# Kernel optimization log

Measured on AMD Instinct MI355X. Metric: run time of the kernel, lower is better.

Reference implementation:

```python
import jax, jax.numpy as jnp
import numpy as np

WINDOW = 16  # window_size from init_kwargs


def sigmoid_cutoff(x):
    # max(min(1.2*sigmoid(x) - 0.1, 1), 0)
    return jnp.clip(1.2 * jax.nn.sigmoid(x) - 0.1, 0.0, 1.0)


def setup_inputs() -> dict:
    key = jax.random.key(0)
    k1, k2, k3 = jax.random.split(key, 3)
    B, S, H = 8, 2048, 1024
    x = jax.random.normal(k1, (B, S, H), dtype=jnp.float32)
    # Dense kernels (glorot-ish scale), x_layer has no bias, y_layer has bias
    Wx = jax.random.normal(k2, (H, H), dtype=jnp.float32) * (1.0 / np.sqrt(H))
    Wy = jax.random.normal(k3, (H, 2 * H), dtype=jnp.float32) * (1.0 / np.sqrt(H))
    by = jnp.zeros((2 * H,), dtype=jnp.float32)
    return {"x": x, "Wx": Wx, "Wy": Wy, "by": by}


def reference(x, Wx, Wy, by):
    B, S, H = x.shape
    # left-pad sequence with window_size-1 zeros, then project once (x_layer)
    xp = jnp.pad(x, ((0, 0), (WINDOW - 1, 0), (0, 0)))
    proj = jnp.einsum('bsh,hd->bsd', xp, Wx)  # [B, S+W-1, H]

    def step(state, i):
        # inputs[:, i:S+i] in the original loop
        inp = jax.lax.dynamic_slice_in_dim(proj, i, S, axis=1)  # [B,S,H]
        ns = jnp.einsum('bsh,hd->bsd', state, Wy) + by          # [B,S,2H]
        # reshape [B,S,2,H]: channel 0 = candidate, channel 1 = gate
        cand, gate_logits = jnp.split(ns, 2, axis=-1)
        gate = sigmoid_cutoff(gate_logits)
        new_state = jax.nn.relu(gate * (inp + cand) + (1.0 - gate) * state)
        return new_state, None

    state0 = jnp.zeros_like(x)
    state, _ = jax.lax.scan(step, state0, jnp.arange(WINDOW))
    return state
```

## Files before the change

kernel.cpp:

```cpp
#include <hip/hip_runtime.h>

#define H 1024
#define SEQ 2048
#define MROWS 16384
#define KD 1024
#define NT32 32
#define EPW 72

typedef _Float16 f16;
typedef _Float16 f16x8 __attribute__((ext_vector_type(8)));
typedef float f32x4 __attribute__((ext_vector_type(4)));

__device__ __forceinline__ float gate_fn(float x) {
    float s = 1.0f / (1.0f + __expf(-x));
    return fminf(fmaxf(1.2f * s - 0.1f, 0.0f), 1.0f);
}

__device__ __forceinline__ void gload_lds16(const void* g, void* lds) {
    __builtin_amdgcn_global_load_lds(
        (const __attribute__((address_space(1))) unsigned int*)g,
        (__attribute__((address_space(3))) unsigned int*)lds, 16, 0, 0);
}

__global__ void k_f32_to_f16(const float* __restrict__ in, f16* __restrict__ out) {
    size_t i = ((size_t)blockIdx.x * blockDim.x + threadIdx.x) * 8;
    float4 v0 = *(const float4*)(in + i);
    float4 v1 = *(const float4*)(in + i + 4);
    f16x8 o;
    o[0] = (f16)v0.x; o[1] = (f16)v0.y; o[2] = (f16)v0.z; o[3] = (f16)v0.w;
    o[4] = (f16)v1.x; o[5] = (f16)v1.y; o[6] = (f16)v1.z; o[7] = (f16)v1.w;
    *(f16x8*)(out + i) = o;
}

__global__ void k_transpose_f16(const float* __restrict__ Wsrc, f16* __restrict__ WT,
                                int K, int N) {
    __shared__ float tile[32][33];
    int n0 = blockIdx.x * 32, k0 = blockIdx.y * 32;
    for (int i = threadIdx.y; i < 32; i += 8)
        tile[i][threadIdx.x] = Wsrc[(size_t)(k0 + i) * N + n0 + threadIdx.x];
    __syncthreads();
    for (int i = threadIdx.y; i < 32; i += 8)
        WT[(size_t)(n0 + i) * K + k0 + threadIdx.x] = (f16)tile[threadIdx.x][i];
}

__global__ __launch_bounds__(256) void k_proj_gemm(const f16* __restrict__ A,
                                                   const f16* __restrict__ BT,
                                                   f16* __restrict__ P16) {
    __shared__ alignas(16) f16 Alds[128 * 32];
    __shared__ alignas(16) f16 Blds[128 * 32];
    const int tid = threadIdx.x;
    const int lane = tid & 63, wid = tid >> 6;
    const int l15 = lane & 15, l4 = lane >> 4;
    const int bm = blockIdx.x, bn = blockIdx.y;

    const f16* gA[2]; const f16* gB[2];
    char* ldsA[2]; char* ldsB[2];
#pragma unroll
    for (int it = 0; it < 2; ++it) {
        int c = it * 4 + wid;
        int row = c * 16 + (lane >> 2);
        int kch = (lane & 3) ^ ((row >> 1) & 3);
        gA[it] = A + (size_t)(bm * 128 + row) * KD + kch * 8;
        gB[it] = BT + (size_t)(bn * 128 + row) * KD + kch * 8;
        ldsA[it] = (char*)Alds + c * 1024;
        ldsB[it] = (char*)Blds + c * 1024;
    }

    int offA[2], offB[8];
#pragma unroll
    for (int m = 0; m < 2; ++m) {
        int row = wid * 32 + m * 16 + l15;
        offA[m] = row * 64 + ((l4 ^ ((row >> 1) & 3)) << 4);
    }
#pragma unroll
    for (int n = 0; n < 8; ++n) {
        int row = n * 16 + l15;
        offB[n] = row * 64 + ((l4 ^ ((row >> 1) & 3)) << 4);
    }

    f32x4 acc[2][8] = {};

    for (int kt = 0; kt < KD / 32; ++kt) {
        __syncthreads();
#pragma unroll
        for (int it = 0; it < 2; ++it) {
            gload_lds16(gA[it], ldsA[it]);
            gload_lds16(gB[it], ldsB[it]);
            gA[it] += 32; gB[it] += 32;
        }
        __syncthreads();
        f16x8 a[2], b[8];
#pragma unroll
        for (int m = 0; m < 2; ++m) a[m] = *(const f16x8*)((const char*)Alds + offA[m]);
#pragma unroll
        for (int n = 0; n < 8; ++n) b[n] = *(const f16x8*)((const char*)Blds + offB[n]);
#pragma unroll
        for (int n = 0; n < 8; ++n)
#pragma unroll
            for (int m = 0; m < 2; ++m)
                acc[m][n] = __builtin_amdgcn_mfma_f32_16x16x32_f16(a[m], b[n], acc[m][n], 0, 0, 0);
    }

#pragma unroll
    for (int m = 0; m < 2; ++m)
#pragma unroll
        for (int n = 0; n < 8; ++n) {
            int col = bn * 128 + n * 16 + l15;
#pragma unroll
            for (int r = 0; r < 4; ++r) {
                int row = bm * 128 + wid * 32 + m * 16 + l4 * 4 + r;
                P16[(size_t)row * H + col] = (f16)acc[m][n][r];
            }
        }
}

__global__ void k_step0(const f16* __restrict__ P16, const float* __restrict__ by,
                        f16* __restrict__ S16) {
    size_t idx = ((size_t)blockIdx.x * blockDim.x + threadIdx.x) * 8;
    int row = (int)(idx >> 10);
    int d = (int)(idx & 1023);
    int s = row & (SEQ - 1);
    f16x8 p = {};
    if (s >= 15) p = *(const f16x8*)(P16 + (size_t)(row - 15) * H + d);
    float4 byc0 = *(const float4*)(by + d);
    float4 byc1 = *(const float4*)(by + d + 4);
    float4 byg0 = *(const float4*)(by + H + d);
    float4 byg1 = *(const float4*)(by + H + d + 4);
    f16x8 sv;
#pragma unroll
    for (int j = 0; j < 8; ++j) {
        float byc = (j < 4) ? ((const float*)&byc0)[j] : ((const float*)&byc1)[j - 4];
        float byg = (j < 4) ? ((const float*)&byg0)[j] : ((const float*)&byg1)[j - 4];
        float g = gate_fn(byg);
        float v = fmaxf(g * ((float)p[j] + byc), 0.f);
        sv[j] = (f16)v;
    }
    *(f16x8*)(S16 + idx) = sv;
}

__global__ __launch_bounds__(512, 4) void k_step_gemm(const f16* __restrict__ A,
                                                      const f16* __restrict__ BT,
                                                      const f16* __restrict__ P16,
                                                      const float* __restrict__ by,
                                                      float* __restrict__ Out,
                                                      f16* __restrict__ Snext,
                                                      int stepi) {
    __shared__ alignas(16) char lds[73728];
    const int tid = threadIdx.x;
    const int lane = tid & 63, w = tid >> 6;
    const int l15 = lane & 15, l4 = lane >> 4;
    const int wr = w >> 1, wc = w & 1;

    const int orig = blockIdx.x;
    const int wg = (orig & 7) * 128 + (orig >> 3);
    const int bm = wg >> 4, tb = wg & 15;

    const int rA0 = w * 16 + (lane >> 2), rA1 = rA0 + 128;
    const int slotA = (lane & 3) ^ ((rA0 >> 1) & 3);
    const char* pA0 = (const char*)A + ((size_t)(bm * 256 + rA0) * KD + slotA * 8) * 2;
    const char* pA1 = (const char*)A + ((size_t)(bm * 256 + rA1) * KD + slotA * 8) * 2;
    const int rB = rA0;
    const int rowB = ((rB & 32) ? H : 0) + tb * 64 + ((rB >> 6) << 5) + (rB & 31);
    const int slotB = (lane & 3) ^ ((rB >> 1) & 3);
    const char* pB = (const char*)BT + ((size_t)rowB * KD + slotB * 8) * 2;
    const int dst = w * 1024 + lane * 16;

#define STAGE(bp) do { \
        gload_lds16(pA0, (bp) + dst); \
        gload_lds16(pA1, (bp) + 8192 + dst); \
        gload_lds16(pB,  (bp) + 16384 + dst); \
        pA0 += 64; pA1 += 64; pB += 64; } while (0)

    const int sx = (l4 ^ ((l15 >> 1) & 3)) << 4;
    int offA[4], offB[4];
#pragma unroll
    for (int m = 0; m < 4; ++m) offA[m] = (wr * 64 + m * 16 + l15) * 64 + sx;
#pragma unroll
    for (int n = 0; n < 4; ++n) offB[n] = 16384 + (wc * 64 + n * 16 + l15) * 64 + sx;

    f32x4 acc[4][4] = {};

    char* cb = lds;
    char* nx = lds + 24576;

    STAGE(cb);
    __syncthreads();

    for (int t = 0; t < NT32; ++t) {
        if (t + 1 < NT32) STAGE(nx);
        f16x8 a[4], b[4];
#pragma unroll
        for (int m = 0; m < 4; ++m) a[m] = *(const f16x8*)(cb + offA[m]);
#pragma unroll
        for (int n = 0; n < 4; ++n) b[n] = *(const f16x8*)(cb + offB[n]);
        __builtin_amdgcn_s_setprio(1);
#pragma unroll
        for (int m = 0; m < 4; ++m)
#pragma unroll
            for (int n = 0; n < 4; ++n)
                acc[m][n] = __builtin_amdgcn_mfma_f32_16x16x32_f16(a[m], b[n], acc[m][n], 0, 0, 0);
        __builtin_amdgcn_s_setprio(0);
        __syncthreads();
        char* tmp = cb; cb = nx; nx = tmp;
    }
#undef STAGE

    const bool last = (stepi == 15);
    f16* Cand = (f16*)lds;
    f16* Gate = (f16*)(lds + 36864);
#pragma unroll
    for (int m = 0; m < 4; ++m)
#pragma unroll
        for (int n = 0; n < 2; ++n)
#pragma unroll
            for (int r4 = 0; r4 < 4; ++r4) {
                int row = wr * 64 + m * 16 + l4 * 4 + r4;
                int cc = wc * 32 + n * 16 + l15;
                Cand[row * EPW + cc] = (f16)acc[m][n][r4];
                Gate[row * EPW + cc] = (f16)acc[m][n + 2][r4];
            }
    __syncthreads();
    {
        const int g = tid & 7;
        const int rb = tid >> 3;
        const int dl = g * 8;
        const int d = tb * 64 + dl;
        float4 byc0 = *(const float4*)(by + d);
        float4 byc1 = *(const float4*)(by + d + 4);
        float4 byg0 = *(const float4*)(by + H + d);
        float4 byg1 = *(const float4*)(by + H + d + 4);
#pragma unroll
        for (int p = 0; p < 4; ++p) {
            int row = p * 64 + rb;
            int grow = bm * 256 + row;
            int s = grow & (SEQ - 1);
            f16x8 c8 = *(const f16x8*)(Cand + row * EPW + dl);
            f16x8 g8 = *(const f16x8*)(Gate + row * EPW + dl);
            f16x8 p8 = {};
            if (s >= 15 - stepi)
                p8 = *(const f16x8*)(P16 + (size_t)(grow + stepi - 15) * H + d);
            f16x8 s8 = *(const f16x8*)(A + (size_t)grow * H + d);
            f16x8 o8; float ov[8];
#pragma unroll
            for (int j = 0; j < 8; ++j) {
                float byc = (j < 4) ? ((const float*)&byc0)[j] : ((const float*)&byc1)[j - 4];
                float byg = (j < 4) ? ((const float*)&byg0)[j] : ((const float*)&byg1)[j - 4];
                float cand = (float)c8[j] + byc;
                float gg = gate_fn((float)g8[j] + byg);
                float v = fmaxf(gg * ((float)p8[j] + cand) + (1.f - gg) * (float)s8[j], 0.f);
                o8[j] = (f16)v; ov[j] = v;
            }
            if (!last) {
                *(f16x8*)(Snext + (size_t)grow * H + d) = o8;
            } else {
                *(float4*)(Out + (size_t)grow * H + d) = make_float4(ov[0], ov[1], ov[2], ov[3]);
                *(float4*)(Out + (size_t)grow * H + d + 4) = make_float4(ov[4], ov[5], ov[6], ov[7]);
            }
        }
    }
}

extern "C" void kernel_launch(void* const* d_in, const int* in_sizes, int n_in,
                              void* d_out, int out_size, void* d_ws, size_t ws_size,
                              hipStream_t stream) {
    (void)in_sizes; (void)n_in; (void)out_size; (void)ws_size;
    const float* x  = (const float*)d_in[0];
    const float* Wx = (const float*)d_in[1];
    const float* Wy = (const float*)d_in[2];
    const float* by = (const float*)d_in[3];
    float* out = (float*)d_out;

    char* ws = (char*)d_ws;
    const size_t MB = 1024ull * 1024ull;
    f16* st16a = (f16*)(ws);
    f16* st16b = (f16*)(ws + 32 * MB);
    f16* P16   = (f16*)(ws + 64 * MB);
    f16* WxT   = (f16*)(ws + 96 * MB);
    f16* WyT   = (f16*)(ws + 98 * MB);

    hipLaunchKernelGGL(k_f32_to_f16, dim3(MROWS * H / 8 / 256), dim3(256), 0, stream, x, st16a);
    hipLaunchKernelGGL(k_transpose_f16, dim3(H / 32, H / 32), dim3(32, 8), 0, stream, Wx, WxT, H, H);
    hipLaunchKernelGGL(k_transpose_f16, dim3(2 * H / 32, H / 32), dim3(32, 8), 0, stream, Wy, WyT, H, 2 * H);
    hipLaunchKernelGGL(k_proj_gemm, dim3(MROWS / 128, H / 128), dim3(256), 0, stream, st16a, WxT, P16);
    hipLaunchKernelGGL(k_step0, dim3(MROWS * H / 8 / 256), dim3(256), 0, stream, P16, by, st16b);

    f16* bufs[2] = {st16a, st16b};
    for (int i = 1; i <= 15; ++i) {
        const f16* cur = bufs[i & 1];
        f16* nxt = bufs[(i + 1) & 1];
        hipLaunchKernelGGL(k_step_gemm, dim3(MROWS / 256 * 16), dim3(512), 0, stream,
                           cur, WyT, P16, by, out, nxt, i);
    }
}
```

Baseline: 1.286 ms.

## Load A fragments directly from global into registers, stage only B through LDS

The step GEMM no longer stages the A tile through LDS. Each wave loads its own A fragments straight from global memory into registers, double-buffered as even/odd register sets, and only the B tile goes through LDS via global_load_lds. This cuts LDS traffic and LDS footprint per stage. The cost is that A rows are read redundantly across the two column waves (wc), with less coalesced global access and more VGPR pressure.

```diff
diff --git a/kernel.cpp b/kernel.cpp
--- a/kernel.cpp
+++ b/kernel.cpp
@@ -155,55 +155,72 @@
     const int wg = (orig & 7) * 128 + (orig >> 3);
     const int bm = wg >> 4, tb = wg & 15;
 
-    const int rA0 = w * 16 + (lane >> 2), rA1 = rA0 + 128;
-    const int slotA = (lane & 3) ^ ((rA0 >> 1) & 3);
-    const char* pA0 = (const char*)A + ((size_t)(bm * 256 + rA0) * KD + slotA * 8) * 2;
-    const char* pA1 = (const char*)A + ((size_t)(bm * 256 + rA1) * KD + slotA * 8) * 2;
-    const int rB = rA0;
+    const int rB = tid >> 2;
     const int rowB = ((rB & 32) ? H : 0) + tb * 64 + ((rB >> 6) << 5) + (rB & 31);
-    const int slotB = (lane & 3) ^ ((rB >> 1) & 3);
+    const int slotB = (tid & 3) ^ ((rB >> 1) & 3);
     const char* pB = (const char*)BT + ((size_t)rowB * KD + slotB * 8) * 2;
-    const int dst = w * 1024 + lane * 16;
-
-#define STAGE(bp) do { \
-        gload_lds16(pA0, (bp) + dst); \
-        gload_lds16(pA1, (bp) + 8192 + dst); \
-        gload_lds16(pB,  (bp) + 16384 + dst); \
-        pA0 += 64; pA1 += 64; pB += 64; } while (0)
+
+    const char* ap[4];
+#pragma unroll
+    for (int m = 0; m < 4; ++m)
+        ap[m] = (const char*)A + ((size_t)(bm * 256 + wr * 64 + m * 16 + l15) * KD + l4 * 8) * 2;
+
+#define STAGEB(bp) do { gload_lds16(pB, (bp) + tid * 16); pB += 64; } while (0)
 
     const int sx = (l4 ^ ((l15 >> 1) & 3)) << 4;
-    int offA[4], offB[4];
-#pragma unroll
-    for (int m = 0; m < 4; ++m) offA[m] = (wr * 64 + m * 16 + l15) * 64 + sx;
-#pragma unroll
-    for (int n = 0; n < 4; ++n) offB[n] = 16384 + (wc * 64 + n * 16 + l15) * 64 + sx;
+    int offB[4];
+#pragma unroll
+    for (int n = 0; n < 4; ++n) offB[n] = (wc * 64 + n * 16 + l15) * 64 + sx;
 
     f32x4 acc[4][4] = {};
-
-    char* cb = lds;
-    char* nx = lds + 24576;
-
-    STAGE(cb);
+    f16x8 aE[4], aO[4];
+
+    char* const buf0 = lds;
+    char* const buf1 = lds + 8192;
+
+    STAGEB(buf0);
+#pragma unroll
+    for (int m = 0; m < 4; ++m) { aE[m] = *(const f16x8*)ap[m]; ap[m] += 64; }
     __syncthreads();
 
-    for (int t = 0; t < NT32; ++t) {
-        if (t + 1 < NT32) STAGE(nx);
-        f16x8 a[4], b[4];
-#pragma unroll
-        for (int m = 0; m < 4; ++m) a[m] = *(const f16x8*)(cb + offA[m]);
-#pragma unroll
-        for (int n = 0; n < 4; ++n) b[n] = *(const f16x8*)(cb + offB[n]);
-        __builtin_amdgcn_s_setprio(1);
-#pragma unroll
-        for (int m = 0; m < 4; ++m)
-#pragma unroll
-            for (int n = 0; n < 4; ++n)
-                acc[m][n] = __builtin_amdgcn_mfma_f32_16x16x32_f16(a[m], b[n], acc[m][n], 0, 0, 0);
-        __builtin_amdgcn_s_setprio(0);
+#pragma unroll 1
+    for (int t = 0; t < NT32; t += 2) {
+        STAGEB(buf1);
+#pragma unroll
+        for (int m = 0; m < 4; ++m) { aO[m] = *(const f16x8*)ap[m]; ap[m] += 64; }
+        {
+            f16x8 b[4];
+#pragma unroll
+            for (int n = 0; n < 4; ++n) b[n] = *(const f16x8*)(buf0 + offB[n]);
+            __builtin_amdgcn_s_setprio(1);
+#pragma unroll
+            for (int m = 0; m < 4; ++m)
+#pragma unroll
+                for (int n = 0; n < 4; ++n)
+                    acc[m][n] = __builtin_amdgcn_mfma_f32_16x16x32_f16(aE[m], b[n], acc[m][n], 0, 0, 0);
+            __builtin_amdgcn_s_setprio(0);
+        }
         __syncthreads();
-        char* tmp = cb; cb = nx; nx = tmp;
-    }
-#undef STAGE
+        if (t + 2 < NT32) {
+            STAGEB(buf0);
+#pragma unroll
+            for (int m = 0; m < 4; ++m) { aE[m] = *(const f16x8*)ap[m]; ap[m] += 64; }
+        }
+        {
+            f16x8 b[4];
+#pragma unroll
+            for (int n = 0; n < 4; ++n) b[n] = *(const f16x8*)(buf1 + offB[n]);
+            __builtin_amdgcn_s_setprio(1);
+#pragma unroll
+            for (int m = 0; m < 4; ++m)
+#pragma unroll
+                for (int n = 0; n < 4; ++n)
+                    acc[m][n] = __builtin_amdgcn_mfma_f32_16x16x32_f16(aO[m], b[n], acc[m][n], 0, 0, 0);
+            __builtin_amdgcn_s_setprio(0);
+        }
+        __syncthreads();
+    }
+#undef STAGEB
 
     const bool last = (stepi == 15);
     f16* Cand = (f16*)lds;
```

Measured after the change: 2.138 ms. 1.66x slower.
